# Performance work log

Measured on AMD Instinct MI355X. Metric: run time of the kernel, lower is better.

The kernel has to match this reference:

```python
import jax, jax.numpy as jnp
import numpy as np

IN_DIM = 256
QK_DIM = IN_DIM // 8


def setup_inputs() -> dict:
    key = jax.random.key(0)
    ks = jax.random.split(key, 6)
    x = jax.random.normal(ks[0], (8, IN_DIM, 64, 64), dtype=jnp.float32)
    # 1x1 conv == per-pixel linear; store weights as [out, in]
    q_w = jax.random.normal(ks[1], (QK_DIM, IN_DIM), dtype=jnp.float32) * (1.0 / np.sqrt(IN_DIM))
    q_b = jax.random.normal(ks[2], (QK_DIM,), dtype=jnp.float32) * 0.01
    v_w = jax.random.normal(ks[3], (IN_DIM, IN_DIM), dtype=jnp.float32) * (1.0 / np.sqrt(IN_DIM))
    v_b = jax.random.normal(ks[4], (IN_DIM,), dtype=jnp.float32) * 0.01
    gamma = jnp.zeros((1,), dtype=jnp.float32) + 0.5  # nonzero so attention branch contributes
    return {"x": x, "q_w": q_w, "q_b": q_b, "v_w": v_w, "v_b": v_b, "gamma": gamma}


def reference(x, q_w, q_b, v_w, v_b, gamma):
    b, c, h, w = x.shape
    n = h * w
    xf = x.reshape(b, c, n)                                    # [b, c, n]
    # NOTE: original forward uses q_conv for BOTH q and k (k_conv unused)
    q = jnp.einsum('oc,bcn->bon', q_w, xf) + q_b[None, :, None]  # [b, d, n]
    proj_q = jnp.transpose(q, (0, 2, 1))                       # [b, n, d]
    energy = jnp.einsum('bid,bdj->bij', proj_q, q)             # [b, n, n]
    attention = jax.nn.softmax(energy, axis=-1)
    v = jnp.einsum('oc,bcn->bon', v_w, xf) + v_b[None, :, None]  # [b, c, n]
    # out[b,c,i] = sum_j v[b,c,j] * attention[b,i,j]
    out = jnp.einsum('bcj,bij->bci', v, attention)
    out = out.reshape(b, c, h, w)
    return gamma * out + x
```

## Files before the change

### kernel.cpp

```cpp
#include <hip/hip_runtime.h>

#define B_   8
#define C_   256
#define D_   32
#define N_   4096
#define FMX  64.0f
#define PSWZ(u) ((u) ^ (((u) >> 3) & 7))
#define VBUF 32768

typedef __attribute__((ext_vector_type(8))) short bf8_t;
typedef __attribute__((ext_vector_type(4))) float f4_t;

__device__ __forceinline__ unsigned short f2bf(float f) {
    unsigned int u = __builtin_bit_cast(unsigned int, f);
    u += 0x7FFFu + ((u >> 16) & 1u);
    return (unsigned short)(u >> 16);
}
__device__ __forceinline__ float bf2f(unsigned short h) {
    unsigned int u = ((unsigned int)h) << 16;
    return __builtin_bit_cast(float, u);
}
__device__ __forceinline__ uint4 pack8(const unsigned short* h) {
    uint4 u;
    u.x = h[0] | ((unsigned)h[1] << 16); u.y = h[2] | ((unsigned)h[3] << 16);
    u.z = h[4] | ((unsigned)h[5] << 16); u.w = h[6] | ((unsigned)h[7] << 16);
    return u;
}
__device__ __forceinline__ void gload_lds16(const void* g, void* l) {
    __builtin_amdgcn_global_load_lds(
        (const __attribute__((address_space(1))) unsigned int*)g,
        (__attribute__((address_space(3))) unsigned int*)l, 16, 0, 0);
}

__global__ __launch_bounds__(256) void wprep_kernel(
    const float* __restrict__ qw, const float* __restrict__ vw,
    unsigned short* __restrict__ wqFh, unsigned short* __restrict__ wqFl,
    unsigned short* __restrict__ wvF)
{
    const int tid = blockIdx.x * 256 + threadIdx.x;
    if (tid < 8192) {
        const int k = tid;
        const int rowblk = k >> 9, kk = (k >> 6) & 7, lane = k & 63;
        const int oc = rowblk * 16 + (lane & 15), c0 = kk * 32 + (lane >> 4) * 8;
        const float* src = vw + oc * 256 + c0;
        unsigned short h[8];
        #pragma unroll
        for (int e = 0; e < 8; ++e) h[e] = f2bf(src[e]);
        *(uint4*)(wvF + (size_t)k * 8) = pack8(h);
    } else if (tid < 9216) {
        const int k = tid - 8192;
        const int rowblk = k >> 9, kk = (k >> 6) & 7, lane = k & 63;
        const int oc = rowblk * 16 + (lane & 15), c0 = kk * 32 + (lane >> 4) * 8;
        const float* src = qw + oc * 256 + c0;
        unsigned short h[8], l[8];
        #pragma unroll
        for (int e = 0; e < 8; ++e) {
            h[e] = f2bf(src[e]);
            l[e] = f2bf(src[e] - bf2f(h[e]));
        }
        *(uint4*)(wqFh + (size_t)k * 8) = pack8(h);
        *(uint4*)(wqFl + (size_t)k * 8) = pack8(l);
    }
}

__global__ __launch_bounds__(256, 4) void proj_kernel(
    const float* __restrict__ x, const unsigned short* __restrict__ wqFh,
    const unsigned short* __restrict__ wqFl, const unsigned short* __restrict__ wvF,
    const float* __restrict__ qb, const float* __restrict__ vb,
    unsigned short* __restrict__ qh, unsigned short* __restrict__ ql,
    unsigned short* __restrict__ vF)
{
    __shared__ __align__(16) unsigned short S[10240];

    const int t    = threadIdx.x;
    const int lane = t & 63;
    const int w    = t >> 6;
    const int q4   = lane >> 4;
    const int l15  = lane & 15;
    const int b    = blockIdx.x & 7;
    const int tt   = blockIdx.x >> 3;
    const int i0   = tt * 32;

    {
        const int n  = lane & 31;
        const int hi = lane >> 5;
        const float* xb = x + (size_t)b * C_ * N_ + i0 + n;
        #pragma unroll
        for (int cc = 0; cc < 4; ++cc) {
            const int chi = w * 8 + cc * 2 + hi;
            float v[8];
            #pragma unroll
            for (int e = 0; e < 8; ++e) v[e] = xb[(size_t)(chi * 8 + e) * N_];
            unsigned short h[8];
            #pragma unroll
            for (int e = 0; e < 8; ++e) h[e] = f2bf(v[e]);
            *(uint4*)&S[(chi * 32 + (n ^ (chi & 3))) * 8] = pack8(h);
        }
    }
    __syncthreads();

    f4_t acc[4][2];
    #pragma unroll
    for (int mt = 0; mt < 4; ++mt)
        #pragma unroll
        for (int nt = 0; nt < 2; ++nt) acc[mt][nt] = (f4_t)0.0f;
    f4_t qacc[2];
    qacc[0] = (f4_t)0.0f; qacc[1] = (f4_t)0.0f;

    #pragma unroll
    for (int kk = 0; kk < 8; ++kk) {
        bf8_t Bh[2];
        #pragma unroll
        for (int nt = 0; nt < 2; ++nt)
            Bh[nt] = *(const bf8_t*)&S[((kk * 4 + q4) * 32 + nt * 16 + (l15 ^ q4)) * 8];
        bf8_t Av[4];
        #pragma unroll
        for (int mt = 0; mt < 4; ++mt)
            Av[mt] = *(const bf8_t*)&wvF[(size_t)(((w * 4 + mt) * 8 + kk) * 64 + lane) * 8];

        #pragma unroll
        for (int mt = 0; mt < 4; ++mt)
            #pragma unroll
            for (int nt = 0; nt < 2; ++nt)
                acc[mt][nt] = __builtin_amdgcn_mfma_f32_16x16x32_bf16(
                    Av[mt], Bh[nt], acc[mt][nt], 0, 0, 0);

        if (w < 2) {
            #pragma unroll
            for (int mq = 0; mq < 2; ++mq) {
                bf8_t Aqh = *(const bf8_t*)&wqFh[(size_t)((mq * 8 + kk) * 64 + lane) * 8];
                bf8_t Aql = *(const bf8_t*)&wqFl[(size_t)((mq * 8 + kk) * 64 + lane) * 8];
                qacc[mq] = __builtin_amdgcn_mfma_f32_16x16x32_bf16(Aqh, Bh[w], qacc[mq], 0, 0, 0);
                qacc[mq] = __builtin_amdgcn_mfma_f32_16x16x32_bf16(Aql, Bh[w], qacc[mq], 0, 0, 0);
            }
        }
    }

    if (w < 2) {
        const int iq = i0 + w * 16 + l15;
        #pragma unroll
        for (int mq = 0; mq < 2; ++mq) {
            float4 qb4 = *(const float4*)(qb + mq * 16 + q4 * 4);
            float qv[4] = {qacc[mq][0] + qb4.x, qacc[mq][1] + qb4.y,
                           qacc[mq][2] + qb4.z, qacc[mq][3] + qb4.w};
            unsigned short hr[4], lr[4];
            #pragma unroll
            for (int r = 0; r < 4; ++r) {
                hr[r] = f2bf(qv[r]);
                lr[r] = f2bf(qv[r] - bf2f(hr[r]));
            }
            uint2 uh, ul;
            uh.x = hr[0] | ((unsigned)hr[1] << 16); uh.y = hr[2] | ((unsigned)hr[3] << 16);
            ul.x = lr[0] | ((unsigned)lr[1] << 16); ul.y = lr[2] | ((unsigned)lr[3] << 16);
            size_t qoff = ((size_t)b * N_ + iq) * D_ + mq * 16 + q4 * 4;
            *(uint2*)(qh + qoff) = uh;
            *(uint2*)(ql + qoff) = ul;
        }
    }

    __syncthreads();
    #pragma unroll
    for (int mt = 0; mt < 4; ++mt) {
        float4 vb4 = *(const float4*)(vb + w * 64 + mt * 16 + q4 * 4);
        float bias[4] = {vb4.x, vb4.y, vb4.z, vb4.w};
        #pragma unroll
        for (int nt = 0; nt < 2; ++nt)
            #pragma unroll
            for (int r = 0; r < 4; ++r)
                S[(w * 64 + mt * 16 + q4 * 4 + r) * 40 + nt * 16 + l15] =
                    f2bf(acc[mt][nt][r] + bias[r]);
    }
    __syncthreads();
    #pragma unroll
    for (int k2 = 0; k2 < 4; ++k2) {
        int id  = k2 * 256 + t;
        int oc  = id >> 2, seg = id & 3;
        uint4 dat = *(const uint4*)&S[oc * 40 + seg * 8];
        size_t p  = (size_t)(tt & 1) * 4 + seg;
        size_t off = ((((size_t)b * 64 + (tt >> 1)) * 8 + p) * 256 + (oc ^ seg)) * 8;
        *(uint4*)(vF + off) = dat;
    }
}

__global__ __launch_bounds__(256, 2) void attn_kernel(
    const unsigned short* __restrict__ qh, const unsigned short* __restrict__ ql,
    const unsigned short* __restrict__ vF, const float* __restrict__ x,
    const float* __restrict__ gamma_p, float* __restrict__ out)
{
    __shared__ __align__(16) unsigned char SMEM[2 * VBUF];
    __shared__ __align__(16) unsigned short Pb[2][4096];
    float* T    = (float*)SMEM;
    float* rowl = (float*)&Pb[0][0];

    const int t    = threadIdx.x;
    const int lane = t & 63;
    const int w    = t >> 6;
    const int q4   = lane >> 4;
    const int l15  = lane & 15;
    const int b    = blockIdx.x & 7;
    const int i0   = (blockIdx.x >> 3) * 64;

    const unsigned short* qhb = qh + (size_t)b * N_ * D_;
    const unsigned short* qlb = ql + (size_t)b * N_ * D_;
    const unsigned short* vFb = vF + (size_t)b * 1048576;

    bf8_t Ah[4], Al[4];
    #pragma unroll
    for (int mt = 0; mt < 4; ++mt) {
        size_t off = (size_t)(i0 + mt * 16 + l15) * D_ + q4 * 8;
        Ah[mt] = *(const bf8_t*)(qhb + off);
        Al[mt] = *(const bf8_t*)(qlb + off);
    }

    auto STAGE = [&](int jt, int buf) {
        const unsigned short* vj = vFb + (size_t)jt * 16384;
        #pragma unroll
        for (int i = 0; i < 8; ++i) {
            const int c = i * 4 + w;
            gload_lds16(vj + c * 512 + lane * 8, &SMEM[buf * VBUF + c * 1024]);
        }
    };

    f4_t acc[4][4];
    #pragma unroll
    for (int mt = 0; mt < 4; ++mt)
        #pragma unroll
        for (int nt = 0; nt < 4; ++nt) acc[mt][nt] = (f4_t)0.0f;

    f4_t lacc[4];
    #pragma unroll
    for (int mt = 0; mt < 4; ++mt) lacc[mt] = (f4_t)0.0f;
    bf8_t onesb;
    #pragma unroll
    for (int e = 0; e < 8; ++e) onesb[e] = (short)0x3F80;

    const int jl = w * 16 + l15;
    const int pprt = jl >> 3, jlo = jl & 7;

    size_t koff0 = (size_t)(w * 16 + l15) * D_ + q4 * 8;
    bf8_t Bh = *(const bf8_t*)(qhb + koff0);
    bf8_t Bl = *(const bf8_t*)(qlb + koff0);
    STAGE(0, 0);

    for (int jt = 0; jt < N_ / 64; ++jt) {
        const int cur = jt & 1;

        f4_t s[4];
        #pragma unroll
        for (int mt = 0; mt < 4; ++mt) {
            f4_t a = (f4_t)0.0f;
            a = __builtin_amdgcn_mfma_f32_16x16x32_bf16(Ah[mt], Bh, a, 0, 0, 0);
            a = __builtin_amdgcn_mfma_f32_16x16x32_bf16(Ah[mt], Bl, a, 0, 0, 0);
            a = __builtin_amdgcn_mfma_f32_16x16x32_bf16(Al[mt], Bh, a, 0, 0, 0);
            s[mt] = a;
        }

        unsigned short pu[4][4];
        #pragma unroll
        for (int mt = 0; mt < 4; ++mt)
            #pragma unroll
            for (int r = 0; r < 4; ++r)
                pu[mt][r] = f2bf(__expf(s[mt][r] - FMX));

        #pragma unroll
        for (int mt = 0; mt < 4; ++mt)
            #pragma unroll
            for (int r = 0; r < 4; ++r) {
                int u = pprt * 64 + mt * 16 + q4 * 4 + r;
                Pb[cur][PSWZ(u) * 8 + jlo] = pu[mt][r];
            }

        __syncthreads();

        const int jn = (jt + 1 < N_ / 64) ? jt + 1 : jt;
        size_t koffn = (size_t)(jn * 64 + w * 16 + l15) * D_ + q4 * 8;
        bf8_t Bh_n = *(const bf8_t*)(qhb + koffn);
        bf8_t Bl_n = *(const bf8_t*)(qlb + koffn);
        if (jt + 1 < N_ / 64) STAGE(jt + 1, cur ^ 1);

        __builtin_amdgcn_s_setprio(1);
        #pragma unroll
        for (int kk = 0; kk < 2; ++kk) {
            bf8_t Af[4], Bf[4];
            #pragma unroll
            for (int nt = 0; nt < 4; ++nt)
                Bf[nt] = *(const bf8_t*)&SMEM[cur * VBUF + (kk * 4 + q4) * 4096 +
                                              ((w * 64 + nt * 16 + l15) ^ q4) * 16];
            #pragma unroll
            for (int mt = 0; mt < 4; ++mt) {
                int u = (kk * 4 + q4) * 64 + mt * 16 + l15;
                Af[mt] = *(const bf8_t*)&Pb[cur][PSWZ(u) * 8];
            }
            #pragma unroll
            for (int mt = 0; mt < 4; ++mt)
                #pragma unroll
                for (int nt = 0; nt < 4; ++nt)
                    acc[mt][nt] = __builtin_amdgcn_mfma_f32_16x16x32_bf16(
                        Af[mt], Bf[nt], acc[mt][nt], 0, 0, 0);
            if (w == 3) {
                #pragma unroll
                for (int mt = 0; mt < 4; ++mt)
                    lacc[mt] = __builtin_amdgcn_mfma_f32_16x16x32_bf16(
                        Af[mt], onesb, lacc[mt], 0, 0, 0);
            }
        }
        __builtin_amdgcn_s_setprio(0);

        Bh = Bh_n; Bl = Bl_n;
    }

    __syncthreads();
    if (w == 3 && l15 == 0) {
        #pragma unroll
        for (int mt = 0; mt < 4; ++mt)
            #pragma unroll
            for (int r = 0; r < 4; ++r)
                rowl[mt * 16 + q4 * 4 + r] = lacc[mt][r];
    }
    __syncthreads();

    const float g = gamma_p[0];
    for (int mt = 0; mt < 4; ++mt) {
        float4 rl = *(float4*)(&rowl[mt * 16 + q4 * 4]);
        float inv[4] = { g / rl.x, g / rl.y, g / rl.z, g / rl.w };
        #pragma unroll
        for (int nt = 0; nt < 4; ++nt)
            #pragma unroll
            for (int r = 0; r < 4; ++r)
                T[(w * 64 + nt * 16 + l15) * 17 + q4 * 4 + r] = acc[mt][nt][r] * inv[r];
        __syncthreads();
        #pragma unroll
        for (int pass = 0; pass < 4; ++pass) {
            int c  = pass * 64 + (t >> 2);
            int ii = (t & 3) * 4;
            float4 o;
            o.x = T[c * 17 + ii];     o.y = T[c * 17 + ii + 1];
            o.z = T[c * 17 + ii + 2]; o.w = T[c * 17 + ii + 3];
            size_t goff = ((size_t)b * C_ + c) * N_ + i0 + mt * 16 + ii;
            float4 xv = *(const float4*)(x + goff);
            o.x += xv.x; o.y += xv.y; o.z += xv.z; o.w += xv.w;
            *(float4*)(out + goff) = o;
        }
        __syncthreads();
    }
}

extern "C" void kernel_launch(void* const* d_in, const int* in_sizes, int n_in,
                              void* d_out, int out_size, void* d_ws, size_t ws_size,
                              hipStream_t stream)
{
    const float* x     = (const float*)d_in[0];
    const float* q_w   = (const float*)d_in[1];
    const float* q_b   = (const float*)d_in[2];
    const float* v_w   = (const float*)d_in[3];
    const float* v_b   = (const float*)d_in[4];
    const float* gamma = (const float*)d_in[5];
    float* out = (float*)d_out;

    unsigned short* ws16 = (unsigned short*)d_ws;
    unsigned short* qhp  = ws16;
    unsigned short* qlp  = ws16 + 1048576;
    unsigned short* vFp  = ws16 + 2097152;
    unsigned short* wvF  = ws16 + 10485760;
    unsigned short* wqFh = wvF + 65536;
    unsigned short* wqFl = wqFh + 8192;

    wprep_kernel<<<36, 256, 0, stream>>>(q_w, v_w, wqFh, wqFl, wvF);
    proj_kernel<<<B_ * (N_ / 32), 256, 0, stream>>>(x, wqFh, wqFl, wvF, q_b, v_b,
                                                    qhp, qlp, vFp);
    attn_kernel<<<B_ * (N_ / 64), 256, 0, stream>>>(qhp, qlp, vFp, x, gamma, out);
}
```

Measured before the change: 225.9 us.

## Unroll attention loop by two with constexpr buffers and precomputed LDS indices

Unrolls the main j-tile loop by two so the double-buffer index becomes a compile-time constant. LDS write and read offsets are precomputed once into registers, and pointer increments replace per-iteration address math. The P-tile swizzle gains an extra XOR term to cut LDS bank conflicts. The s_setprio hints are dropped and the next K fragment is loaded straight into Bh/Bl instead of temporaries, which could shorten the prefetch distance and costs more registers.

```diff
diff --git a/kernel.cpp b/kernel.cpp
--- a/kernel.cpp
+++ b/kernel.cpp
@@ -5,7 +5,7 @@
 #define D_   32
 #define N_   4096
 #define FMX  64.0f
-#define PSWZ(u) ((u) ^ (((u) >> 3) & 7))
+#define PSWZ2(u) ((u) ^ (((u) >> 3) & 7) ^ ((((u) >> 6) & 3) << 1))
 #define VBUF 32768
 
 typedef __attribute__((ext_vector_type(8))) short bf8_t;
@@ -31,6 +31,9 @@
         (const __attribute__((address_space(1))) unsigned int*)g,
         (__attribute__((address_space(3))) unsigned int*)l, 16, 0, 0);
 }
+
+struct IC0 { static constexpr int v = 0; };
+struct IC1 { static constexpr int v = 1; };
 
 __global__ __launch_bounds__(256) void wprep_kernel(
     const float* __restrict__ qw, const float* __restrict__ vw,
@@ -212,38 +215,65 @@
         Al[mt] = *(const bf8_t*)(qlb + off);
     }
 
-    auto STAGE = [&](int jt, int buf) {
-        const unsigned short* vj = vFb + (size_t)jt * 16384;
+    const int jl = w * 16 + l15;
+    const int pprt = jl >> 3, jlo = jl & 7;
+    int pwIdx[4][4];
+    #pragma unroll
+    for (int mt = 0; mt < 4; ++mt)
+        #pragma unroll
+        for (int r = 0; r < 4; ++r) {
+            int u = pprt * 64 + mt * 16 + q4 * 4 + r;
+            pwIdx[mt][r] = PSWZ2(u) * 8 + jlo;
+        }
+    int rdIdx[2][4];
+    #pragma unroll
+    for (int kk = 0; kk < 2; ++kk)
+        #pragma unroll
+        for (int mt = 0; mt < 4; ++mt) {
+            int u = (kk * 4 + q4) * 64 + mt * 16 + l15;
+            rdIdx[kk][mt] = PSWZ2(u) * 8;
+        }
+    int bfOff[2][4];
+    #pragma unroll
+    for (int kk = 0; kk < 2; ++kk)
+        #pragma unroll
+        for (int nt = 0; nt < 4; ++nt)
+            bfOff[kk][nt] = (kk * 4 + q4) * 4096 +
+                            ((w * 64 + nt * 16 + l15) ^ q4) * 16;
+
+    f4_t acc[4][4];
+    #pragma unroll
+    for (int mt = 0; mt < 4; ++mt)
+        #pragma unroll
+        for (int nt = 0; nt < 4; ++nt) acc[mt][nt] = (f4_t)0.0f;
+
+    f4_t lacc[4];
+    #pragma unroll
+    for (int mt = 0; mt < 4; ++mt) lacc[mt] = (f4_t)0.0f;
+    bf8_t onesb;
+    #pragma unroll
+    for (int e = 0; e < 8; ++e) onesb[e] = (short)0x3F80;
+
+    const int koffBase = jl * D_ + q4 * 8;
+    const unsigned short* khp = qhb + 2048 + koffBase;
+    const unsigned short* klp = qlb + 2048 + koffBase;
+    const unsigned short* vjp = vFb + 16384;
+
+    bf8_t Bh = *(const bf8_t*)(qhb + koffBase);
+    bf8_t Bl = *(const bf8_t*)(qlb + koffBase);
+    {
+        const unsigned short* vj = vFb;
         #pragma unroll
         for (int i = 0; i < 8; ++i) {
             const int c = i * 4 + w;
-            gload_lds16(vj + c * 512 + lane * 8, &SMEM[buf * VBUF + c * 1024]);
-        }
-    };
-
-    f4_t acc[4][4];
-    #pragma unroll
-    for (int mt = 0; mt < 4; ++mt)
-        #pragma unroll
-        for (int nt = 0; nt < 4; ++nt) acc[mt][nt] = (f4_t)0.0f;
-
-    f4_t lacc[4];
-    #pragma unroll
-    for (int mt = 0; mt < 4; ++mt) lacc[mt] = (f4_t)0.0f;
-    bf8_t onesb;
-    #pragma unroll
-    for (int e = 0; e < 8; ++e) onesb[e] = (short)0x3F80;
-
-    const int jl = w * 16 + l15;
-    const int pprt = jl >> 3, jlo = jl & 7;
-
-    size_t koff0 = (size_t)(w * 16 + l15) * D_ + q4 * 8;
-    bf8_t Bh = *(const bf8_t*)(qhb + koff0);
-    bf8_t Bl = *(const bf8_t*)(qlb + koff0);
-    STAGE(0, 0);
-
-    for (int jt = 0; jt < N_ / 64; ++jt) {
-        const int cur = jt & 1;
+            gload_lds16(vj + c * 512 + lane * 8, &SMEM[c * 1024]);
+        }
+    }
+
+    auto body = [&](int jt, auto ic) {
+        constexpr int cur = decltype(ic)::v;
+        unsigned short* Pbc = &Pb[cur][0];
+        const unsigned char* Vsc = &SMEM[cur * VBUF];
 
         f4_t s[4];
         #pragma unroll
@@ -255,42 +285,36 @@
             s[mt] = a;
         }
 
-        unsigned short pu[4][4];
         #pragma unroll
         for (int mt = 0; mt < 4; ++mt)
             #pragma unroll
             for (int r = 0; r < 4; ++r)
-                pu[mt][r] = f2bf(__expf(s[mt][r] - FMX));
-
-        #pragma unroll
-        for (int mt = 0; mt < 4; ++mt)
-            #pragma unroll
-            for (int r = 0; r < 4; ++r) {
-                int u = pprt * 64 + mt * 16 + q4 * 4 + r;
-                Pb[cur][PSWZ(u) * 8 + jlo] = pu[mt][r];
+                Pbc[pwIdx[mt][r]] = f2bf(__expf(s[mt][r] - FMX));
+
+        __syncthreads();
+
+        if (jt + 1 < N_ / 64) {
+            Bh = *(const bf8_t*)khp;
+            Bl = *(const bf8_t*)klp;
+            khp += 2048; klp += 2048;
+            #pragma unroll
+            for (int i = 0; i < 8; ++i) {
+                const int c = i * 4 + w;
+                gload_lds16(vjp + c * 512 + lane * 8,
+                            &SMEM[(cur ^ 1) * VBUF + c * 1024]);
             }
-
-        __syncthreads();
-
-        const int jn = (jt + 1 < N_ / 64) ? jt + 1 : jt;
-        size_t koffn = (size_t)(jn * 64 + w * 16 + l15) * D_ + q4 * 8;
-        bf8_t Bh_n = *(const bf8_t*)(qhb + koffn);
-        bf8_t Bl_n = *(const bf8_t*)(qlb + koffn);
-        if (jt + 1 < N_ / 64) STAGE(jt + 1, cur ^ 1);
-
-        __builtin_amdgcn_s_setprio(1);
+            vjp += 16384;
+        }
+
         #pragma unroll
         for (int kk = 0; kk < 2; ++kk) {
             bf8_t Af[4], Bf[4];
             #pragma unroll
             for (int nt = 0; nt < 4; ++nt)
-                Bf[nt] = *(const bf8_t*)&SMEM[cur * VBUF + (kk * 4 + q4) * 4096 +
-                                              ((w * 64 + nt * 16 + l15) ^ q4) * 16];
-            #pragma unroll
-            for (int mt = 0; mt < 4; ++mt) {
-                int u = (kk * 4 + q4) * 64 + mt * 16 + l15;
-                Af[mt] = *(const bf8_t*)&Pb[cur][PSWZ(u) * 8];
-            }
+                Bf[nt] = *(const bf8_t*)&Vsc[bfOff[kk][nt]];
+            #pragma unroll
+            for (int mt = 0; mt < 4; ++mt)
+                Af[mt] = *(const bf8_t*)&Pbc[rdIdx[kk][mt]];
             #pragma unroll
             for (int mt = 0; mt < 4; ++mt)
                 #pragma unroll
@@ -304,9 +328,11 @@
                         Af[mt], onesb, lacc[mt], 0, 0, 0);
             }
         }
-        __builtin_amdgcn_s_setprio(0);
-
-        Bh = Bh_n; Bl = Bl_n;
+    };
+
+    for (int jtp = 0; jtp < N_ / 64; jtp += 2) {
+        body(jtp,     IC0{});
+        body(jtp + 1, IC1{});
     }
 
     __syncthreads();
```

Result: faster. 217.3 us (-3.8%).
